# Performance work log

Hardware: AMD Instinct MI355X
Metric: run time of the kernel (lower is better)

Reference implementation:

```python
import jax, jax.numpy as jnp
import numpy as np

N_NODES = 100000
N_EDGES = 1600000
IN_CH = 64
HID = 64
OUT = 2


def sage_conv(x, src, dst, W_agg, W_root, b):
    # PyG SAGEConv (mean aggr): out = lin_l(mean_{j in N(i)} x_j) + lin_r(x_i)
    n = x.shape[0]
    msgs = x[src]                                        # [E, F] gather
    agg = jax.ops.segment_sum(msgs, dst, num_segments=n)  # [N, F] scatter-add
    cnt = jax.ops.segment_sum(jnp.ones((src.shape[0], 1), x.dtype), dst, num_segments=n)
    agg = agg / jnp.maximum(cnt, 1)                      # mean; isolated nodes -> 0
    return agg @ W_agg + x @ W_root + b


def setup_inputs() -> dict:
    key = jax.random.key(0)
    ks = jax.random.split(key, 8)
    s = lambda f: 1.0 / np.sqrt(f)
    x = jax.random.normal(ks[0], (N_NODES, IN_CH), dtype=jnp.float32)
    edge_index = jax.random.randint(ks[1], (2, N_EDGES), 0, N_NODES, dtype=jnp.int64)
    return {
        "x": x,
        "edge_index": edge_index,
        "W1_agg": jax.random.normal(ks[2], (IN_CH, HID), dtype=jnp.float32) * s(IN_CH),
        "W1_root": jax.random.normal(ks[3], (IN_CH, HID), dtype=jnp.float32) * s(IN_CH),
        "b1": jnp.zeros((HID,), jnp.float32),
        "W2_agg": jax.random.normal(ks[4], (HID, HID), dtype=jnp.float32) * s(HID),
        "W2_root": jax.random.normal(ks[5], (HID, HID), dtype=jnp.float32) * s(HID),
        "b2": jnp.zeros((HID,), jnp.float32),
        "W_lin": jax.random.normal(ks[6], (HID, OUT), dtype=jnp.float32) * s(HID),
        "b_lin": jnp.zeros((OUT,), jnp.float32),
    }


def reference(x, edge_index, W1_agg, W1_root, b1, W2_agg, W2_root, b2, W_lin, b_lin):
    src, dst = edge_index[0], edge_index[1]
    h = jax.nn.relu(sage_conv(x, src, dst, W1_agg, W1_root, b1))   # dropout = identity (eval)
    h = jax.nn.relu(sage_conv(h, src, dst, W2_agg, W2_root, b2))
    return h @ W_lin + b_lin
```

## Files before the change

kernel.cpp:

```cpp
#include <hip/hip_runtime.h>
#include <hip/hip_bf16.h>

#define FEAT 64
#define CHUNK 2048
#define MAX_NB 1024

typedef __attribute__((ext_vector_type(8))) short bf16x8;
typedef __attribute__((ext_vector_type(4))) float f32x4;
typedef __attribute__((ext_vector_type(2))) float f32x2;

__device__ __forceinline__ float bflo2f(unsigned int u) {
    union { unsigned int u; float f; } v; v.u = u << 16; return v.f;
}
__device__ __forceinline__ float bfhi2f(unsigned int u) {
    union { unsigned int u; float f; } v; v.u = u & 0xffff0000u; return v.f;
}
__device__ __forceinline__ unsigned short f2bf(float f) {
    union { float f; unsigned int u; } v; v.f = f;
    unsigned int u = v.u;
    u += 0x7fffu + ((u >> 16) & 1u);
    return (unsigned short)(u >> 16);
}
__device__ __forceinline__ f32x2 bfpair(unsigned int u) {
    f32x2 r; r.x = bflo2f(u & 0xffffu); r.y = bfhi2f(u); return r;
}

__global__ __launch_bounds__(256) void prep_p1_kernel(
    const unsigned short* __restrict__ xh, const int* __restrict__ ei32,
    const void* __restrict__ w1a, const void* __restrict__ w1r,
    const void* __restrict__ b1,  const void* __restrict__ w2a,
    const void* __restrict__ w2r, const void* __restrict__ b2,
    const void* __restrict__ wl,  const void* __restrict__ bl,
    float* __restrict__ wbuf, unsigned short* __restrict__ Wt,
    int* __restrict__ flags, const void* __restrict__ x_in,
    unsigned short* __restrict__ x16, int n8,
    int* __restrict__ hist, int E, int N, int NB, int EC, int pB) {
    __shared__ int lh[MAX_NB];
    __shared__ int cnt_bf, cnt_nz;
    int tid = threadIdx.x;

    if (blockIdx.x >= pB) {
        int c = blockIdx.x - pB;
        if (tid == 0) cnt_nz = 0;
        for (int i = tid; i < NB; i += 256) lh[i] = 0;
        __syncthreads();
        if (ei32[tid * 2 + 1] != 0) atomicAdd(&cnt_nz, 1);
        __syncthreads();
        int idx64 = (cnt_nz < 8) ? 1 : 0;
        long base = (long)c * CHUNK;
#pragma unroll 4
        for (int j = 0; j < CHUNK / 256; ++j) {
            long e = base + j * 256 + tid;
            if (e < E) {
                int d = idx64 ? ei32[2 * ((long)E + e)] : ei32[(long)E + e];
                if ((unsigned)d < (unsigned)N)
                    atomicAdd(&lh[d >> 8], 1);
            }
        }
        __syncthreads();
        for (int k = tid; k < NB; k += 256) hist[(long)k * EC + c] = lh[k];
        return;
    }

    if (tid == 0) { cnt_bf = 0; cnt_nz = 0; }
    __syncthreads();
    unsigned short h = xh[tid * 2];
    int e = (h >> 7) & 0xFF;
    if (e >= 110 && e <= 132) atomicAdd(&cnt_bf, 1);
    if (ei32[tid * 2 + 1] != 0) atomicAdd(&cnt_nz, 1);
    __syncthreads();
    int f0 = (cnt_bf >= 128) ? 1 : 0;
    if (blockIdx.x == 0 && tid == 0) {
        flags[0] = f0;
        flags[1] = (cnt_nz < 8) ? 1 : 0;
    }
    int i = blockIdx.x * 256 + tid;
    if (i < 16642) {
        const void* src; int off;
        if      (i < 4096)  { src = w1a; off = i; }
        else if (i < 8192)  { src = w1r; off = i - 4096; }
        else if (i < 8256)  { src = b1;  off = i - 8192; }
        else if (i < 12352) { src = w2a; off = i - 8256; }
        else if (i < 16448) { src = w2r; off = i - 12352; }
        else if (i < 16512) { src = b2;  off = i - 16448; }
        else if (i < 16640) { src = wl;  off = i - 16512; }
        else                { src = bl;  off = i - 16640; }
        float v = f0 ? bflo2f(((const unsigned short*)src)[off])
                     : ((const float*)src)[off];
        wbuf[i] = v;
        unsigned short hv = f2bf(v);
        if (i < 4096)                      Wt[(off & 63) * 128 + (off >> 6)] = hv;
        else if (i < 8192)                 Wt[(off & 63) * 128 + 64 + (off >> 6)] = hv;
        else if (i >= 8256 && i < 12352)   Wt[8192 + (off & 63) * 128 + (off >> 6)] = hv;
        else if (i >= 12352 && i < 16448)  Wt[8192 + (off & 63) * 128 + 64 + (off >> 6)] = hv;
    }
    if (!f0 && i < n8) {
        float4 a = ((const float4*)x_in)[2 * i];
        float4 b = ((const float4*)x_in)[2 * i + 1];
        uint4 o;
        o.x = (unsigned int)f2bf(a.x) | ((unsigned int)f2bf(a.y) << 16);
        o.y = (unsigned int)f2bf(a.z) | ((unsigned int)f2bf(a.w) << 16);
        o.z = (unsigned int)f2bf(b.x) | ((unsigned int)f2bf(b.y) << 16);
        o.w = (unsigned int)f2bf(b.z) | ((unsigned int)f2bf(b.w) << 16);
        ((uint4*)x16)[i] = o;
    }
}

__global__ __launch_bounds__(256) void scan1_kernel(const int* __restrict__ in,
                                                    int* __restrict__ out,
                                                    int* __restrict__ blocksum, int n) {
    int tid = threadIdx.x;
    int base = blockIdx.x * 2048 + tid * 8;
    int v[8];
    int tsum = 0;
#pragma unroll
    for (int i = 0; i < 8; ++i) {
        v[i] = (base + i < n) ? in[base + i] : 0;
        tsum += v[i];
    }
    int lane = tid & 63;
    int x = tsum;
#pragma unroll
    for (int off = 1; off < 64; off <<= 1) {
        int y = __shfl_up(x, off);
        if (lane >= off) x += y;
    }
    __shared__ int wsum[4];
    int wave = tid >> 6;
    if (lane == 63) wsum[wave] = x;
    __syncthreads();
    int woff = 0;
#pragma unroll
    for (int w = 0; w < 4; ++w) if (w < wave) woff += wsum[w];
    int run = woff + x - tsum;
#pragma unroll
    for (int i = 0; i < 8; ++i) {
        if (base + i < n) out[base + i] = run;
        run += v[i];
    }
    if (tid == 255) blocksum[blockIdx.x] = woff + x;
}

__global__ __launch_bounds__(256) void scan3_kernel(int* __restrict__ out,
                                                    const int* __restrict__ blocksum, int n) {
    int bb = blockIdx.x, tid = threadIdx.x;
    __shared__ int wsum[4];
    __shared__ int spre;
    int s = 0;
    for (int b = tid; b < bb; b += 256) s += blocksum[b];
#pragma unroll
    for (int off = 32; off > 0; off >>= 1) s += __shfl_down(s, off);
    int lane = tid & 63, wave = tid >> 6;
    if (lane == 0) wsum[wave] = s;
    __syncthreads();
    if (tid == 0) spre = wsum[0] + wsum[1] + wsum[2] + wsum[3];
    __syncthreads();
    int pre = spre;
    int base = bb * 2048;
#pragma unroll
    for (int k = 0; k < 8; ++k) {
        int i = base + k * 256 + tid;
        if (i < n) out[i] += pre;
    }
}

__global__ __launch_bounds__(256) void p3_scatter_kernel(
    const int* __restrict__ ei32, const int* __restrict__ hscan,
    int* __restrict__ bkt, int E, int N, int NB, int EC,
    const int* __restrict__ flags) {
    __shared__ int lh[MAX_NB];
    int tid = threadIdx.x, c = blockIdx.x;
    for (int i = tid; i < NB; i += 256) lh[i] = 0;
    __syncthreads();
    int idx64 = flags[1];
    long base = (long)c * CHUNK;
#pragma unroll 4
    for (int j = 0; j < CHUNK / 256; ++j) {
        long e = base + j * 256 + tid;
        if (e < E) {
            int s = idx64 ? ei32[2 * e]             : ei32[e];
            int d = idx64 ? ei32[2 * ((long)E + e)] : ei32[(long)E + e];
            if ((unsigned)d < (unsigned)N) {
                if ((unsigned)s >= (unsigned)N) s = 0;
                int k = d >> 8;
                int r = atomicAdd(&lh[k], 1);
                bkt[hscan[(long)k * EC + c] + r] = s | ((d & 255) << 20);
            }
        }
    }
}

__global__ __launch_bounds__(256) void p4_build_kernel(
    const int* __restrict__ bkt, const int* __restrict__ hscan, const int* __restrict__ hist,
    int* __restrict__ offs, int* __restrict__ cnt, int* __restrict__ srcs,
    int E, int N, int NB, int EC) {
    int k = blockIdx.x, tid = threadIdx.x;
    int start = hscan[(long)k * EC];
    int end = (k + 1 < NB) ? hscan[(long)(k + 1) * EC]
                           : (hscan[(long)NB * EC - 1] + hist[(long)NB * EC - 1]);
    __shared__ int lc[256], lheads[256], wsum[4];
    lc[tid] = 0;
    __syncthreads();
    for (int e = start + tid; e < end; e += 256)
        atomicAdd(&lc[(bkt[e] >> 20) & 255], 1);
    __syncthreads();
    int cv = lc[tid];
    int lane = tid & 63, wave = tid >> 6;
    int x = cv;
#pragma unroll
    for (int off = 1; off < 64; off <<= 1) {
        int y = __shfl_up(x, off);
        if (lane >= off) x += y;
    }
    if (lane == 63) wsum[wave] = x;
    __syncthreads();
    int woff = 0;
#pragma unroll
    for (int w = 0; w < 4; ++w) if (w < wave) woff += wsum[w];
    int excl = woff + x - cv;
    int gnode = k * 256 + tid;
    if (gnode < N) { offs[gnode] = start + excl; cnt[gnode] = cv; }
    lheads[tid] = excl;
    __syncthreads();
    for (int e = start + tid; e < end; e += 256) {
        int p = bkt[e];
        int d8 = (p >> 20) & 255;
        int pos = start + atomicAdd(&lheads[d8], 1);
        srcs[pos] = p & 0xFFFFF;
    }
}

__global__ __launch_bounds__(256) void sage_fused_kernel(
    const void* __restrict__ feat_raw, const unsigned short* __restrict__ feat_ws,
    const int* __restrict__ srcs, const int* __restrict__ offs,
    const int* __restrict__ cnt,
    const unsigned short* __restrict__ Wt, const float* __restrict__ bias,
    unsigned short* __restrict__ out16, int N,
    const float* __restrict__ wl, const float* __restrict__ bl,
    void* __restrict__ out_final, const int* __restrict__ flags, int sel) {

    const unsigned short* feat16 =
        (sel && !flags[0]) ? feat_ws : (const unsigned short*)feat_raw;

    __shared__ unsigned short A_l[64][72];
    __shared__ unsigned short B_l[64][136];

    int tid = threadIdx.x;
    int blk = blockIdx.x;

#pragma unroll
    for (int i = 0; i < 4; ++i) {
        int ch = tid + i * 256;
        int n = ch >> 4, kc = ch & 15;
        *(uint4*)&B_l[n][kc * 8] = *(const uint4*)(Wt + n * 128 + kc * 8);
    }

    int lane = tid & 63;
    int wave = tid >> 6;
    int g = lane >> 3;
    int li = lane & 7;

    for (int pass = 0; pass < 2; ++pass) {
        int r = pass * 32 + wave * 8 + g;
        int node = blk * 64 + r;
        f32x2 a0 = {0.f, 0.f}, a1 = a0, a2 = a0, a3 = a0;
        int deg = 0;
        if (node < N) {
            int start = offs[node];
            deg = cnt[node];
            int j = 0;
            for (; j + 4 <= deg; j += 4) {
                int s0 = srcs[start + j];
                int s1 = srcs[start + j + 1];
                int s2 = srcs[start + j + 2];
                int s3 = srcs[start + j + 3];
                uint4 u0 = *(const uint4*)(feat16 + (size_t)s0 * FEAT + 8 * li);
                uint4 u1 = *(const uint4*)(feat16 + (size_t)s1 * FEAT + 8 * li);
                uint4 u2 = *(const uint4*)(feat16 + (size_t)s2 * FEAT + 8 * li);
                uint4 u3 = *(const uint4*)(feat16 + (size_t)s3 * FEAT + 8 * li);
                a0 += bfpair(u0.x); a1 += bfpair(u0.y); a2 += bfpair(u0.z); a3 += bfpair(u0.w);
                a0 += bfpair(u1.x); a1 += bfpair(u1.y); a2 += bfpair(u1.z); a3 += bfpair(u1.w);
                a0 += bfpair(u2.x); a1 += bfpair(u2.y); a2 += bfpair(u2.z); a3 += bfpair(u2.w);
                a0 += bfpair(u3.x); a1 += bfpair(u3.y); a2 += bfpair(u3.z); a3 += bfpair(u3.w);
            }
            for (; j < deg; ++j) {
                int s = srcs[start + j];
                uint4 u = *(const uint4*)(feat16 + (size_t)s * FEAT + 8 * li);
                a0 += bfpair(u.x); a1 += bfpair(u.y); a2 += bfpair(u.z); a3 += bfpair(u.w);
            }
        }
        float inv = 1.0f / (float)(deg > 0 ? deg : 1);
        uint4 o;
        o.x = (unsigned)f2bf(a0.x * inv) | ((unsigned)f2bf(a0.y * inv) << 16);
        o.y = (unsigned)f2bf(a1.x * inv) | ((unsigned)f2bf(a1.y * inv) << 16);
        o.z = (unsigned)f2bf(a2.x * inv) | ((unsigned)f2bf(a2.y * inv) << 16);
        o.w = (unsigned)f2bf(a3.x * inv) | ((unsigned)f2bf(a3.y * inv) << 16);
        *(uint4*)&A_l[r][8 * li] = o;
    }
    __syncthreads();

    int r0 = wave * 16;
    int m = lane & 15, quad = lane >> 4;

    int arow = blk * 64 + r0 + m;
    if (arow >= N) arow = 0;
    const unsigned short* rootp = feat16 + (size_t)arow * FEAT + quad * 8;

    f32x4 acc0 = {0.f, 0.f, 0.f, 0.f};
    f32x4 acc1 = acc0, acc2 = acc0, acc3 = acc0;

#pragma unroll
    for (int k0 = 0; k0 < 128; k0 += 32) {
        bf16x8 a;
        if (k0 < 64) a = *(const bf16x8*)&A_l[r0 + m][k0 + quad * 8];
        else         a = *(const bf16x8*)(rootp + (k0 - 64));
        bf16x8 b0 = *(const bf16x8*)&B_l[ 0 + m][k0 + quad * 8];
        bf16x8 b1 = *(const bf16x8*)&B_l[16 + m][k0 + quad * 8];
        bf16x8 b2 = *(const bf16x8*)&B_l[32 + m][k0 + quad * 8];
        bf16x8 b3 = *(const bf16x8*)&B_l[48 + m][k0 + quad * 8];
        acc0 = __builtin_amdgcn_mfma_f32_16x16x32_bf16(a, b0, acc0, 0, 0, 0);
        acc1 = __builtin_amdgcn_mfma_f32_16x16x32_bf16(a, b1, acc1, 0, 0, 0);
        acc2 = __builtin_amdgcn_mfma_f32_16x16x32_bf16(a, b2, acc2, 0, 0, 0);
        acc3 = __builtin_amdgcn_mfma_f32_16x16x32_bf16(a, b3, acc3, 0, 0, 0);
    }
    __syncthreads();

#pragma unroll
    for (int c = 0; c < 4; ++c) {
        f32x4 av = (c == 0) ? acc0 : (c == 1) ? acc1 : (c == 2) ? acc2 : acc3;
        float bv = bias[c * 16 + m];
#pragma unroll
        for (int reg = 0; reg < 4; ++reg) {
            float v = fmaxf(av[reg] + bv, 0.f);
            A_l[r0 + quad * 4 + reg][c * 16 + m] = f2bf(v);
        }
    }
    __syncthreads();

    if (out16) {
#pragma unroll
        for (int i = 0; i < 2; ++i) {
            int ch = tid + i * 256;
            int r = ch >> 3, c = ch & 7;
            int row = blk * 64 + r;
            if (row < N)
                ((uint4*)(out16 + (size_t)row * FEAT))[c] = *(const uint4*)&A_l[r][c * 8];
        }
    }

    if (wl) {
        int r = tid >> 2, part = tid & 3;
        int row = blk * 64 + r;
        if (row < N) {
            float p0 = 0.f, p1 = 0.f;
#pragma unroll
            for (int j = 0; j < 16; ++j) {
                int f = part * 16 + j;
                float v = bflo2f(A_l[r][f]);
                p0 += v * wl[f * 2 + 0];
                p1 += v * wl[f * 2 + 1];
            }
            p0 += __shfl_down(p0, 2, 4); p0 += __shfl_down(p0, 1, 4);
            p1 += __shfl_down(p1, 2, 4); p1 += __shfl_down(p1, 1, 4);
            if (part == 0) {
                p0 += bl[0];
                p1 += bl[1];
                if (flags[0]) {
                    unsigned int o = ((unsigned int)f2bf(p1) << 16) | (unsigned int)f2bf(p0);
                    ((unsigned int*)out_final)[row] = o;
                } else {
                    ((float2*)out_final)[row] = make_float2(p0, p1);
                }
            }
        }
    }
}

extern "C" void kernel_launch(void* const* d_in, const int* in_sizes, int n_in,
                              void* d_out, int out_size, void* d_ws, size_t ws_size,
                              hipStream_t stream) {
    const void* x_in = d_in[0];
    const int*  ei32 = (const int*)d_in[1];

    int N = in_sizes[0] / FEAT;
    int E = in_sizes[1] / 2;
    int NB = (N + 255) >> 8;
    int EC = (E + CHUNK - 1) / CHUNK;
    int HN = NB * EC;

    unsigned short* x16   = (unsigned short*)d_ws;
    unsigned short* h16   = x16 + (size_t)N * FEAT;
    unsigned short* Wt    = h16 + (size_t)N * FEAT;
    float*          wbuf  = (float*)(Wt + 16384);
    int*            hist  = (int*)(wbuf + 16704);
    int*            hscan = hist + HN;
    int*            bsum  = hscan + HN;
    int*            flags = bsum + 1024;
    int*            offs  = flags + 16;
    int*            cnt   = offs + N;
    int*            bkt   = cnt + N;
    int*            srcs  = bkt + E;

    float* b1_32 = wbuf + 8192;
    float* b2_32 = wbuf + 16448;
    float* wl32  = wbuf + 16512;
    float* bl32  = wbuf + 16640;

    int n8 = N * FEAT / 8;
    int pBlocks = (n8 + 255) / 256;
    if (pBlocks < 66) pBlocks = 66;
    prep_p1_kernel<<<pBlocks + EC, 256, 0, stream>>>(
        (const unsigned short*)x_in, ei32,
        d_in[2], d_in[3], d_in[4], d_in[5], d_in[6], d_in[7], d_in[8], d_in[9],
        wbuf, Wt, flags, x_in, x16, n8,
        hist, E, N, NB, EC, pBlocks);

    int sB = (HN + 2047) / 2048;
    scan1_kernel<<<sB, 256, 0, stream>>>(hist, hscan, bsum, HN);
    scan3_kernel<<<sB, 256, 0, stream>>>(hscan, bsum, HN);
    p3_scatter_kernel<<<EC, 256, 0, stream>>>(ei32, hscan, bkt, E, N, NB, EC, flags);
    p4_build_kernel<<<NB, 256, 0, stream>>>(bkt, hscan, hist, offs, cnt, srcs, E, N, NB, EC);

    int gBlocks = (N + 63) / 64;

    sage_fused_kernel<<<gBlocks, 256, 0, stream>>>(
        x_in, x16, srcs, offs, cnt, Wt, b1_32, h16, N,
        nullptr, nullptr, nullptr, flags, 1);

    sage_fused_kernel<<<gBlocks, 256, 0, stream>>>(
        h16, h16, srcs, offs, cnt, Wt + 8192, b2_32, nullptr, N,
        wl32, bl32, d_out, flags, 0);
}
```

Before: 231.4 us.

## Replace two-level bucket CSR build with global atomic count and scatter

Replaces the bucketed histogram, scatter and per-bucket build passes with a direct per-node degree count using global atomics, a scan over node counts, and a single atomic-cursor scatter of source indices. This removes one kernel launch and the intermediate bucket array. In exchange it issues global atomics per edge twice onto random addresses, and the neighbour order within each node becomes nondeterministic, which can change floating-point summation order.

Measured after the change: 400.8 us. 1.73x slower.

```diff
diff --git a/kernel.cpp b/kernel.cpp
--- a/kernel.cpp
+++ b/kernel.cpp
@@ -2,8 +2,7 @@
 #include <hip/hip_bf16.h>
 
 #define FEAT 64
-#define CHUNK 2048
-#define MAX_NB 1024
+#define CHUNK 8192
 
 typedef __attribute__((ext_vector_type(8))) short bf16x8;
 typedef __attribute__((ext_vector_type(4))) float f32x4;
@@ -25,7 +24,7 @@
     f32x2 r; r.x = bflo2f(u & 0xffffu); r.y = bfhi2f(u); return r;
 }
 
-__global__ __launch_bounds__(256) void prep_p1_kernel(
+__global__ __launch_bounds__(256) void prep_count_kernel(
     const unsigned short* __restrict__ xh, const int* __restrict__ ei32,
     const void* __restrict__ w1a, const void* __restrict__ w1r,
     const void* __restrict__ b1,  const void* __restrict__ w2a,
@@ -34,15 +33,13 @@
     float* __restrict__ wbuf, unsigned short* __restrict__ Wt,
     int* __restrict__ flags, const void* __restrict__ x_in,
     unsigned short* __restrict__ x16, int n8,
-    int* __restrict__ hist, int E, int N, int NB, int EC, int pB) {
-    __shared__ int lh[MAX_NB];
+    int* __restrict__ cnt_g, int E, int N, int pB) {
     __shared__ int cnt_bf, cnt_nz;
     int tid = threadIdx.x;
 
     if (blockIdx.x >= pB) {
         int c = blockIdx.x - pB;
         if (tid == 0) cnt_nz = 0;
-        for (int i = tid; i < NB; i += 256) lh[i] = 0;
         __syncthreads();
         if (ei32[tid * 2 + 1] != 0) atomicAdd(&cnt_nz, 1);
         __syncthreads();
@@ -54,11 +51,9 @@
             if (e < E) {
                 int d = idx64 ? ei32[2 * ((long)E + e)] : ei32[(long)E + e];
                 if ((unsigned)d < (unsigned)N)
-                    atomicAdd(&lh[d >> 8], 1);
-            }
-        }
-        __syncthreads();
-        for (int k = tid; k < NB; k += 256) hist[(long)k * EC + c] = lh[k];
+                    atomicAdd(&cnt_g[d], 1);
+            }
+        }
         return;
     }
 
@@ -142,6 +137,7 @@
 }
 
 __global__ __launch_bounds__(256) void scan3_kernel(int* __restrict__ out,
+                                                    int* __restrict__ head,
                                                     const int* __restrict__ blocksum, int n) {
     int bb = blockIdx.x, tid = threadIdx.x;
     __shared__ int wsum[4];
@@ -160,73 +156,27 @@
 #pragma unroll
     for (int k = 0; k < 8; ++k) {
         int i = base + k * 256 + tid;
-        if (i < n) out[i] += pre;
-    }
-}
-
-__global__ __launch_bounds__(256) void p3_scatter_kernel(
-    const int* __restrict__ ei32, const int* __restrict__ hscan,
-    int* __restrict__ bkt, int E, int N, int NB, int EC,
-    const int* __restrict__ flags) {
-    __shared__ int lh[MAX_NB];
-    int tid = threadIdx.x, c = blockIdx.x;
-    for (int i = tid; i < NB; i += 256) lh[i] = 0;
-    __syncthreads();
+        if (i < n) {
+            int v = out[i] + pre;
+            out[i] = v;
+            head[i] = v;
+        }
+    }
+}
+
+__global__ __launch_bounds__(256) void scatter_kernel(
+    const int* __restrict__ ei32, int* __restrict__ head,
+    int* __restrict__ srcs, int E, int N, const int* __restrict__ flags) {
     int idx64 = flags[1];
-    long base = (long)c * CHUNK;
-#pragma unroll 4
-    for (int j = 0; j < CHUNK / 256; ++j) {
-        long e = base + j * 256 + tid;
-        if (e < E) {
-            int s = idx64 ? ei32[2 * e]             : ei32[e];
-            int d = idx64 ? ei32[2 * ((long)E + e)] : ei32[(long)E + e];
-            if ((unsigned)d < (unsigned)N) {
-                if ((unsigned)s >= (unsigned)N) s = 0;
-                int k = d >> 8;
-                int r = atomicAdd(&lh[k], 1);
-                bkt[hscan[(long)k * EC + c] + r] = s | ((d & 255) << 20);
-            }
-        }
-    }
-}
-
-__global__ __launch_bounds__(256) void p4_build_kernel(
-    const int* __restrict__ bkt, const int* __restrict__ hscan, const int* __restrict__ hist,
-    int* __restrict__ offs, int* __restrict__ cnt, int* __restrict__ srcs,
-    int E, int N, int NB, int EC) {
-    int k = blockIdx.x, tid = threadIdx.x;
-    int start = hscan[(long)k * EC];
-    int end = (k + 1 < NB) ? hscan[(long)(k + 1) * EC]
-                           : (hscan[(long)NB * EC - 1] + hist[(long)NB * EC - 1]);
-    __shared__ int lc[256], lheads[256], wsum[4];
-    lc[tid] = 0;
-    __syncthreads();
-    for (int e = start + tid; e < end; e += 256)
-        atomicAdd(&lc[(bkt[e] >> 20) & 255], 1);
-    __syncthreads();
-    int cv = lc[tid];
-    int lane = tid & 63, wave = tid >> 6;
-    int x = cv;
-#pragma unroll
-    for (int off = 1; off < 64; off <<= 1) {
-        int y = __shfl_up(x, off);
-        if (lane >= off) x += y;
-    }
-    if (lane == 63) wsum[wave] = x;
-    __syncthreads();
-    int woff = 0;
-#pragma unroll
-    for (int w = 0; w < 4; ++w) if (w < wave) woff += wsum[w];
-    int excl = woff + x - cv;
-    int gnode = k * 256 + tid;
-    if (gnode < N) { offs[gnode] = start + excl; cnt[gnode] = cv; }
-    lheads[tid] = excl;
-    __syncthreads();
-    for (int e = start + tid; e < end; e += 256) {
-        int p = bkt[e];
-        int d8 = (p >> 20) & 255;
-        int pos = start + atomicAdd(&lheads[d8], 1);
-        srcs[pos] = p & 0xFFFFF;
+    long stride = (long)gridDim.x * 256;
+    for (long e = (long)blockIdx.x * 256 + threadIdx.x; e < E; e += stride) {
+        int s = idx64 ? ei32[2 * e]             : ei32[e];
+        int d = idx64 ? ei32[2 * ((long)E + e)] : ei32[(long)E + e];
+        if ((unsigned)d < (unsigned)N) {
+            if ((unsigned)s >= (unsigned)N) s = 0;
+            int pos = atomicAdd(&head[d], 1);
+            srcs[pos] = s;
+        }
     }
 }
 
@@ -384,42 +334,42 @@
 
     int N = in_sizes[0] / FEAT;
     int E = in_sizes[1] / 2;
-    int NB = (N + 255) >> 8;
-    int EC = (E + CHUNK - 1) / CHUNK;
-    int HN = NB * EC;
 
     unsigned short* x16   = (unsigned short*)d_ws;
     unsigned short* h16   = x16 + (size_t)N * FEAT;
     unsigned short* Wt    = h16 + (size_t)N * FEAT;
     float*          wbuf  = (float*)(Wt + 16384);
-    int*            hist  = (int*)(wbuf + 16704);
-    int*            hscan = hist + HN;
-    int*            bsum  = hscan + HN;
-    int*            flags = bsum + 1024;
-    int*            offs  = flags + 16;
-    int*            cnt   = offs + N;
-    int*            bkt   = cnt + N;
-    int*            srcs  = bkt + E;
+    int*            flags = (int*)(wbuf + 16704);
+    int*            bsum  = flags + 16;
+    int*            cnt   = bsum + 1024;
+    int*            offs  = cnt + N;
+    int*            head  = offs + N;
+    int*            srcs  = head + N;
 
     float* b1_32 = wbuf + 8192;
     float* b2_32 = wbuf + 16448;
     float* wl32  = wbuf + 16512;
     float* bl32  = wbuf + 16640;
 
+    hipMemsetAsync(cnt, 0, (size_t)N * sizeof(int), stream);
+
     int n8 = N * FEAT / 8;
     int pBlocks = (n8 + 255) / 256;
     if (pBlocks < 66) pBlocks = 66;
-    prep_p1_kernel<<<pBlocks + EC, 256, 0, stream>>>(
+    int cB = (E + CHUNK - 1) / CHUNK;
+    prep_count_kernel<<<pBlocks + cB, 256, 0, stream>>>(
         (const unsigned short*)x_in, ei32,
         d_in[2], d_in[3], d_in[4], d_in[5], d_in[6], d_in[7], d_in[8], d_in[9],
         wbuf, Wt, flags, x_in, x16, n8,
-        hist, E, N, NB, EC, pBlocks);
-
-    int sB = (HN + 2047) / 2048;
-    scan1_kernel<<<sB, 256, 0, stream>>>(hist, hscan, bsum, HN);
-    scan3_kernel<<<sB, 256, 0, stream>>>(hscan, bsum, HN);
-    p3_scatter_kernel<<<EC, 256, 0, stream>>>(ei32, hscan, bkt, E, N, NB, EC, flags);
-    p4_build_kernel<<<NB, 256, 0, stream>>>(bkt, hscan, hist, offs, cnt, srcs, E, N, NB, EC);
+        cnt, E, N, pBlocks);
+
+    int sB = (N + 2047) / 2048;
+    scan1_kernel<<<sB, 256, 0, stream>>>(cnt, offs, bsum, N);
+    scan3_kernel<<<sB, 256, 0, stream>>>(offs, head, bsum, N);
+
+    int scB = (E + 255) / 256;
+    if (scB > 2048) scB = 2048;
+    scatter_kernel<<<scB, 256, 0, stream>>>(ei32, head, srcs, E, N, flags);
 
     int gBlocks = (N + 63) / 64;
 
```

## Merge CSR-building kernels into one cooperative kernel with grid syncs

Applied to the files above, without the earlier changes.

The five CSR-construction launches (prep/histogram, two scan passes, bucket scatter, per-bucket build) are replaced by a single cooperative kernel on a fixed 512-block grid, with grid-wide syncs between phases. The aim is to remove launch gaps and tail effects between the small dependent kernels. A fallback path of separate kernels runs if the cooperative launch is unavailable. In exchange, the persistent grid loops over chunks with fewer blocks than before (EC is about 782 chunks), grid.sync has its own cost, and the unroll pragmas were dropped.

Result: slower. 511.9 us (+121.2%).

```diff
diff --git a/kernel.cpp b/kernel.cpp
--- a/kernel.cpp
+++ b/kernel.cpp
@@ -1,9 +1,13 @@
 #include <hip/hip_runtime.h>
 #include <hip/hip_bf16.h>
+#include <hip/hip_cooperative_groups.h>
 
 #define FEAT 64
 #define CHUNK 2048
 #define MAX_NB 1024
+#define MEGA_GRID 512
+
+namespace cg = cooperative_groups;
 
 typedef __attribute__((ext_vector_type(8))) short bf16x8;
 typedef __attribute__((ext_vector_type(4))) float f32x4;
@@ -25,56 +29,13 @@
     f32x2 r; r.x = bflo2f(u & 0xffffu); r.y = bfhi2f(u); return r;
 }
 
-__global__ __launch_bounds__(256) void prep_p1_kernel(
-    const unsigned short* __restrict__ xh, const int* __restrict__ ei32,
-    const void* __restrict__ w1a, const void* __restrict__ w1r,
-    const void* __restrict__ b1,  const void* __restrict__ w2a,
-    const void* __restrict__ w2r, const void* __restrict__ b2,
-    const void* __restrict__ wl,  const void* __restrict__ bl,
-    float* __restrict__ wbuf, unsigned short* __restrict__ Wt,
-    int* __restrict__ flags, const void* __restrict__ x_in,
-    unsigned short* __restrict__ x16, int n8,
-    int* __restrict__ hist, int E, int N, int NB, int EC, int pB) {
-    __shared__ int lh[MAX_NB];
-    __shared__ int cnt_bf, cnt_nz;
-    int tid = threadIdx.x;
-
-    if (blockIdx.x >= pB) {
-        int c = blockIdx.x - pB;
-        if (tid == 0) cnt_nz = 0;
-        for (int i = tid; i < NB; i += 256) lh[i] = 0;
-        __syncthreads();
-        if (ei32[tid * 2 + 1] != 0) atomicAdd(&cnt_nz, 1);
-        __syncthreads();
-        int idx64 = (cnt_nz < 8) ? 1 : 0;
-        long base = (long)c * CHUNK;
-#pragma unroll 4
-        for (int j = 0; j < CHUNK / 256; ++j) {
-            long e = base + j * 256 + tid;
-            if (e < E) {
-                int d = idx64 ? ei32[2 * ((long)E + e)] : ei32[(long)E + e];
-                if ((unsigned)d < (unsigned)N)
-                    atomicAdd(&lh[d >> 8], 1);
-            }
-        }
-        __syncthreads();
-        for (int k = tid; k < NB; k += 256) hist[(long)k * EC + c] = lh[k];
-        return;
-    }
-
-    if (tid == 0) { cnt_bf = 0; cnt_nz = 0; }
-    __syncthreads();
-    unsigned short h = xh[tid * 2];
-    int e = (h >> 7) & 0xFF;
-    if (e >= 110 && e <= 132) atomicAdd(&cnt_bf, 1);
-    if (ei32[tid * 2 + 1] != 0) atomicAdd(&cnt_nz, 1);
-    __syncthreads();
-    int f0 = (cnt_bf >= 128) ? 1 : 0;
-    if (blockIdx.x == 0 && tid == 0) {
-        flags[0] = f0;
-        flags[1] = (cnt_nz < 8) ? 1 : 0;
-    }
-    int i = blockIdx.x * 256 + tid;
+
+__device__ __forceinline__ void phase_prep_elem(
+    int i, int f0,
+    const void* w1a, const void* w1r, const void* b1, const void* w2a,
+    const void* w2r, const void* b2, const void* wl, const void* bl,
+    float* wbuf, unsigned short* Wt,
+    const void* x_in, unsigned short* x16, int n8) {
     if (i < 16642) {
         const void* src; int off;
         if      (i < 4096)  { src = w1a; off = i; }
@@ -106,18 +67,32 @@
     }
 }
 
-__global__ __launch_bounds__(256) void scan1_kernel(const int* __restrict__ in,
-                                                    int* __restrict__ out,
-                                                    int* __restrict__ blocksum, int n) {
-    int tid = threadIdx.x;
-    int base = blockIdx.x * 2048 + tid * 8;
+__device__ __forceinline__ void phase_hist_chunk(
+    int c, int idx64, const int* __restrict__ ei32, int* __restrict__ hist,
+    int E, int N, int NB, int EC, int* lh, int tid) {
+    for (int i = tid; i < NB; i += 256) lh[i] = 0;
+    __syncthreads();
+    long base = (long)c * CHUNK;
+    for (int j = 0; j < CHUNK / 256; ++j) {
+        long e = base + j * 256 + tid;
+        if (e < E) {
+            int d = idx64 ? ei32[2 * ((long)E + e)] : ei32[(long)E + e];
+            if ((unsigned)d < (unsigned)N) atomicAdd(&lh[d >> 8], 1);
+        }
+    }
+    __syncthreads();
+    for (int k = tid; k < NB; k += 256) hist[(long)k * EC + c] = lh[k];
+    __syncthreads();
+}
+
+__device__ __forceinline__ void phase_scan1_block(
+    int b, const int* __restrict__ in, int* __restrict__ out,
+    int* __restrict__ bsum, int n, int tid, int* sh) {
+    int base = b * 2048 + tid * 8;
     int v[8];
     int tsum = 0;
 #pragma unroll
-    for (int i = 0; i < 8; ++i) {
-        v[i] = (base + i < n) ? in[base + i] : 0;
-        tsum += v[i];
-    }
+    for (int i = 0; i < 8; ++i) { v[i] = (base + i < n) ? in[base + i] : 0; tsum += v[i]; }
     int lane = tid & 63;
     int x = tsum;
 #pragma unroll
@@ -125,56 +100,47 @@
         int y = __shfl_up(x, off);
         if (lane >= off) x += y;
     }
-    __shared__ int wsum[4];
     int wave = tid >> 6;
-    if (lane == 63) wsum[wave] = x;
+    if (lane == 63) sh[wave] = x;
     __syncthreads();
     int woff = 0;
 #pragma unroll
-    for (int w = 0; w < 4; ++w) if (w < wave) woff += wsum[w];
+    for (int w = 0; w < 4; ++w) if (w < wave) woff += sh[w];
     int run = woff + x - tsum;
 #pragma unroll
-    for (int i = 0; i < 8; ++i) {
-        if (base + i < n) out[base + i] = run;
-        run += v[i];
-    }
-    if (tid == 255) blocksum[blockIdx.x] = woff + x;
-}
-
-__global__ __launch_bounds__(256) void scan3_kernel(int* __restrict__ out,
-                                                    const int* __restrict__ blocksum, int n) {
-    int bb = blockIdx.x, tid = threadIdx.x;
-    __shared__ int wsum[4];
-    __shared__ int spre;
+    for (int i = 0; i < 8; ++i) { if (base + i < n) out[base + i] = run; run += v[i]; }
+    if (tid == 255) bsum[b] = woff + x;
+    __syncthreads();
+}
+
+__device__ __forceinline__ void phase_scan3_block(
+    int b, int* __restrict__ out, const int* __restrict__ bsum,
+    int n, int tid, int* sh) {
     int s = 0;
-    for (int b = tid; b < bb; b += 256) s += blocksum[b];
+    for (int q = tid; q < b; q += 256) s += bsum[q];
 #pragma unroll
     for (int off = 32; off > 0; off >>= 1) s += __shfl_down(s, off);
     int lane = tid & 63, wave = tid >> 6;
-    if (lane == 0) wsum[wave] = s;
-    __syncthreads();
-    if (tid == 0) spre = wsum[0] + wsum[1] + wsum[2] + wsum[3];
-    __syncthreads();
-    int pre = spre;
-    int base = bb * 2048;
+    if (lane == 0) sh[wave] = s;
+    __syncthreads();
+    if (tid == 0) sh[4] = sh[0] + sh[1] + sh[2] + sh[3];
+    __syncthreads();
+    int pre = sh[4];
+    int base = b * 2048;
 #pragma unroll
     for (int k = 0; k < 8; ++k) {
         int i = base + k * 256 + tid;
         if (i < n) out[i] += pre;
     }
-}
-
-__global__ __launch_bounds__(256) void p3_scatter_kernel(
-    const int* __restrict__ ei32, const int* __restrict__ hscan,
-    int* __restrict__ bkt, int E, int N, int NB, int EC,
-    const int* __restrict__ flags) {
-    __shared__ int lh[MAX_NB];
-    int tid = threadIdx.x, c = blockIdx.x;
+    __syncthreads();
+}
+
+__device__ __forceinline__ void phase_p3_chunk(
+    int c, int idx64, const int* __restrict__ ei32, const int* __restrict__ hscan,
+    int* __restrict__ bkt, int E, int N, int NB, int EC, int* lh, int tid) {
     for (int i = tid; i < NB; i += 256) lh[i] = 0;
     __syncthreads();
-    int idx64 = flags[1];
     long base = (long)c * CHUNK;
-#pragma unroll 4
     for (int j = 0; j < CHUNK / 256; ++j) {
         long e = base + j * 256 + tid;
         if (e < E) {
@@ -188,17 +154,17 @@
             }
         }
     }
-}
-
-__global__ __launch_bounds__(256) void p4_build_kernel(
-    const int* __restrict__ bkt, const int* __restrict__ hscan, const int* __restrict__ hist,
-    int* __restrict__ offs, int* __restrict__ cnt, int* __restrict__ srcs,
-    int E, int N, int NB, int EC) {
-    int k = blockIdx.x, tid = threadIdx.x;
+    __syncthreads();
+}
+
+__device__ __forceinline__ void phase_p4_bucket(
+    int k, const int* __restrict__ bkt, const int* __restrict__ hscan,
+    const int* __restrict__ hist, int* __restrict__ offs, int* __restrict__ cnt,
+    int* __restrict__ srcs, int N, int NB, int EC, int* sh, int tid) {
+    int* lc = sh; int* lheads = sh + 256; int* wsum = sh + 512;
     int start = hscan[(long)k * EC];
     int end = (k + 1 < NB) ? hscan[(long)(k + 1) * EC]
                            : (hscan[(long)NB * EC - 1] + hist[(long)NB * EC - 1]);
-    __shared__ int lc[256], lheads[256], wsum[4];
     lc[tid] = 0;
     __syncthreads();
     for (int e = start + tid; e < end; e += 256)
@@ -228,6 +194,105 @@
         int pos = start + atomicAdd(&lheads[d8], 1);
         srcs[pos] = p & 0xFFFFF;
     }
+    __syncthreads();
+}
+
+__global__ __launch_bounds__(256) void csr_mega_kernel(
+    const unsigned short* __restrict__ xh, const int* __restrict__ ei32,
+    const void* w1a, const void* w1r, const void* b1, const void* w2a,
+    const void* w2r, const void* b2, const void* wl, const void* bl,
+    float* __restrict__ wbuf, unsigned short* __restrict__ Wt, int* __restrict__ flags,
+    const void* __restrict__ x_in, unsigned short* __restrict__ x16, int n8, int pMax,
+    int* __restrict__ hist, int* __restrict__ hscan, int* __restrict__ bsum,
+    int* __restrict__ offs, int* __restrict__ cnt, int* __restrict__ bkt,
+    int* __restrict__ srcs,
+    int E, int N, int NB, int EC, int HN, int sB) {
+    cg::grid_group grid = cg::this_grid();
+    __shared__ int sh[MAX_NB];
+    int tid = threadIdx.x;
+
+    if (tid == 0) { sh[0] = 0; sh[1] = 0; }
+    __syncthreads();
+    if (ei32[tid * 2 + 1] != 0) atomicAdd(&sh[0], 1);
+    { unsigned short h = xh[tid * 2]; int e = (h >> 7) & 0xFF;
+      if (e >= 110 && e <= 132) atomicAdd(&sh[1], 1); }
+    __syncthreads();
+    int idx64 = (sh[0] < 8) ? 1 : 0;
+    int f0 = (sh[1] >= 128) ? 1 : 0;
+    if (blockIdx.x == 0 && tid == 0) { flags[0] = f0; flags[1] = idx64; }
+    __syncthreads();
+
+    for (int i = blockIdx.x * 256 + tid; i < pMax; i += gridDim.x * 256)
+        phase_prep_elem(i, f0, w1a, w1r, b1, w2a, w2r, b2, wl, bl,
+                        wbuf, Wt, x_in, x16, n8);
+
+    for (int c = blockIdx.x; c < EC; c += gridDim.x)
+        phase_hist_chunk(c, idx64, ei32, hist, E, N, NB, EC, sh, tid);
+    grid.sync();
+
+    if (blockIdx.x < sB) phase_scan1_block(blockIdx.x, hist, hscan, bsum, HN, tid, sh);
+    grid.sync();
+
+    if (blockIdx.x < sB) phase_scan3_block(blockIdx.x, hscan, bsum, HN, tid, sh);
+    grid.sync();
+
+    for (int c = blockIdx.x; c < EC; c += gridDim.x)
+        phase_p3_chunk(c, idx64, ei32, hscan, bkt, E, N, NB, EC, sh, tid);
+    grid.sync();
+
+    for (int k = blockIdx.x; k < NB; k += gridDim.x)
+        phase_p4_bucket(k, bkt, hscan, hist, offs, cnt, srcs, N, NB, EC, sh, tid);
+}
+
+__global__ __launch_bounds__(256) void fb_prep_kernel(
+    const unsigned short* __restrict__ xh, const int* __restrict__ ei32,
+    const void* w1a, const void* w1r, const void* b1, const void* w2a,
+    const void* w2r, const void* b2, const void* wl, const void* bl,
+    float* __restrict__ wbuf, unsigned short* __restrict__ Wt, int* __restrict__ flags,
+    const void* __restrict__ x_in, unsigned short* __restrict__ x16, int n8, int pMax) {
+    __shared__ int c0, c1;
+    int tid = threadIdx.x;
+    if (tid == 0) { c0 = 0; c1 = 0; }
+    __syncthreads();
+    if (ei32[tid * 2 + 1] != 0) atomicAdd(&c0, 1);
+    { unsigned short h = xh[tid * 2]; int e = (h >> 7) & 0xFF;
+      if (e >= 110 && e <= 132) atomicAdd(&c1, 1); }
+    __syncthreads();
+    int f0 = (c1 >= 128) ? 1 : 0;
+    if (blockIdx.x == 0 && tid == 0) { flags[0] = f0; flags[1] = (c0 < 8) ? 1 : 0; }
+    int i = blockIdx.x * 256 + tid;
+    if (i < pMax)
+        phase_prep_elem(i, f0, w1a, w1r, b1, w2a, w2r, b2, wl, bl,
+                        wbuf, Wt, x_in, x16, n8);
+}
+__global__ __launch_bounds__(256) void fb_hist_kernel(
+    const int* __restrict__ ei32, int* __restrict__ hist,
+    int E, int N, int NB, int EC, const int* __restrict__ flags) {
+    __shared__ int sh[MAX_NB];
+    phase_hist_chunk(blockIdx.x, flags[1], ei32, hist, E, N, NB, EC, sh, threadIdx.x);
+}
+__global__ __launch_bounds__(256) void fb_scan1_kernel(
+    const int* __restrict__ in, int* __restrict__ out, int* __restrict__ bsum, int n) {
+    __shared__ int sh[8];
+    phase_scan1_block(blockIdx.x, in, out, bsum, n, threadIdx.x, sh);
+}
+__global__ __launch_bounds__(256) void fb_scan3_kernel(
+    int* __restrict__ out, const int* __restrict__ bsum, int n) {
+    __shared__ int sh[8];
+    phase_scan3_block(blockIdx.x, out, bsum, n, threadIdx.x, sh);
+}
+__global__ __launch_bounds__(256) void fb_p3_kernel(
+    const int* __restrict__ ei32, const int* __restrict__ hscan, int* __restrict__ bkt,
+    int E, int N, int NB, int EC, const int* __restrict__ flags) {
+    __shared__ int sh[MAX_NB];
+    phase_p3_chunk(blockIdx.x, flags[1], ei32, hscan, bkt, E, N, NB, EC, sh, threadIdx.x);
+}
+__global__ __launch_bounds__(256) void fb_p4_kernel(
+    const int* __restrict__ bkt, const int* __restrict__ hscan,
+    const int* __restrict__ hist, int* __restrict__ offs, int* __restrict__ cnt,
+    int* __restrict__ srcs, int N, int NB, int EC) {
+    __shared__ int sh[520];
+    phase_p4_bucket(blockIdx.x, bkt, hscan, hist, offs, cnt, srcs, N, NB, EC, sh, threadIdx.x);
 }
 
 __global__ __launch_bounds__(256) void sage_fused_kernel(
@@ -381,12 +446,18 @@
                               hipStream_t stream) {
     const void* x_in = d_in[0];
     const int*  ei32 = (const int*)d_in[1];
+    const unsigned short* xh = (const unsigned short*)x_in;
+    const void* w1a = d_in[2]; const void* w1r = d_in[3];
+    const void* b1p = d_in[4]; const void* w2a = d_in[5];
+    const void* w2r = d_in[6]; const void* b2p = d_in[7];
+    const void* wlp = d_in[8]; const void* blp = d_in[9];
 
     int N = in_sizes[0] / FEAT;
     int E = in_sizes[1] / 2;
     int NB = (N + 255) >> 8;
     int EC = (E + CHUNK - 1) / CHUNK;
     int HN = NB * EC;
+    int sB = (HN + 2047) / 2048;
 
     unsigned short* x16   = (unsigned short*)d_ws;
     unsigned short* h16   = x16 + (size_t)N * FEAT;
@@ -407,19 +478,36 @@
     float* bl32  = wbuf + 16640;
 
     int n8 = N * FEAT / 8;
-    int pBlocks = (n8 + 255) / 256;
-    if (pBlocks < 66) pBlocks = 66;
-    prep_p1_kernel<<<pBlocks + EC, 256, 0, stream>>>(
-        (const unsigned short*)x_in, ei32,
-        d_in[2], d_in[3], d_in[4], d_in[5], d_in[6], d_in[7], d_in[8], d_in[9],
-        wbuf, Wt, flags, x_in, x16, n8,
-        hist, E, N, NB, EC, pBlocks);
-
-    int sB = (HN + 2047) / 2048;
-    scan1_kernel<<<sB, 256, 0, stream>>>(hist, hscan, bsum, HN);
-    scan3_kernel<<<sB, 256, 0, stream>>>(hscan, bsum, HN);
-    p3_scatter_kernel<<<EC, 256, 0, stream>>>(ei32, hscan, bkt, E, N, NB, EC, flags);
-    p4_build_kernel<<<NB, 256, 0, stream>>>(bkt, hscan, hist, offs, cnt, srcs, E, N, NB, EC);
+    int pMax = (n8 > 16642) ? n8 : 16642;
+
+    bool coop = false;
+    int occ = 0;
+    if (hipOccupancyMaxActiveBlocksPerMultiprocessor(&occ, csr_mega_kernel, 256, 0)
+            == hipSuccess && occ >= 2) {
+        void* args[] = {
+            (void*)&xh, (void*)&ei32,
+            (void*)&w1a, (void*)&w1r, (void*)&b1p, (void*)&w2a,
+            (void*)&w2r, (void*)&b2p, (void*)&wlp, (void*)&blp,
+            (void*)&wbuf, (void*)&Wt, (void*)&flags,
+            (void*)&x_in, (void*)&x16, (void*)&n8, (void*)&pMax,
+            (void*)&hist, (void*)&hscan, (void*)&bsum,
+            (void*)&offs, (void*)&cnt, (void*)&bkt, (void*)&srcs,
+            (void*)&E, (void*)&N, (void*)&NB, (void*)&EC, (void*)&HN, (void*)&sB };
+        if (hipLaunchCooperativeKernel(csr_mega_kernel, dim3(MEGA_GRID), dim3(256),
+                                       args, 0, stream) == hipSuccess)
+            coop = true;
+    }
+    if (!coop) {
+        int pBlocks = (pMax + 255) / 256;
+        fb_prep_kernel<<<pBlocks, 256, 0, stream>>>(
+            xh, ei32, w1a, w1r, b1p, w2a, w2r, b2p, wlp, blp,
+            wbuf, Wt, flags, x_in, x16, n8, pMax);
+        fb_hist_kernel<<<EC, 256, 0, stream>>>(ei32, hist, E, N, NB, EC, flags);
+        fb_scan1_kernel<<<sB, 256, 0, stream>>>(hist, hscan, bsum, HN);
+        fb_scan3_kernel<<<sB, 256, 0, stream>>>(hscan, bsum, HN);
+        fb_p3_kernel<<<EC, 256, 0, stream>>>(ei32, hscan, bkt, E, N, NB, EC, flags);
+        fb_p4_kernel<<<NB, 256, 0, stream>>>(bkt, hscan, hist, offs, cnt, srcs, N, NB, EC);
+    }
 
     int gBlocks = (N + 63) / 64;
 
```

## Merge two-pass histogram scan into single-pass chained scan, enlarge edge chunks

Applied to the files above, without the earlier changes.

Replaces the two scan kernels with one kernel in which each block publishes its block total through a flag and spins on all earlier blocks' flags to build its prefix. This removes one kernel launch and a second pass over the histogram. The edge chunk size grows from 2048 to 8192, so there are four times fewer histogram columns and scatter blocks, but each block does more serial work and has less parallelism. The chained scan assumes earlier blocks get scheduled first; with the small grid this is likely safe, but it is a forward-progress risk.

Result: slower. 243.7 us (+5.3%).

```diff
diff --git a/kernel.cpp b/kernel.cpp
--- a/kernel.cpp
+++ b/kernel.cpp
@@ -2,7 +2,7 @@
 #include <hip/hip_bf16.h>
 
 #define FEAT 64
-#define CHUNK 2048
+#define CHUNK 8192
 #define MAX_NB 1024
 
 typedef __attribute__((ext_vector_type(8))) short bf16x8;
@@ -34,7 +34,8 @@
     float* __restrict__ wbuf, unsigned short* __restrict__ Wt,
     int* __restrict__ flags, const void* __restrict__ x_in,
     unsigned short* __restrict__ x16, int n8,
-    int* __restrict__ hist, int E, int N, int NB, int EC, int pB) {
+    int* __restrict__ hist, int* __restrict__ bflag, int sB,
+    int E, int N, int NB, int EC, int pB) {
     __shared__ int lh[MAX_NB];
     __shared__ int cnt_bf, cnt_nz;
     int tid = threadIdx.x;
@@ -70,9 +71,12 @@
     if (ei32[tid * 2 + 1] != 0) atomicAdd(&cnt_nz, 1);
     __syncthreads();
     int f0 = (cnt_bf >= 128) ? 1 : 0;
-    if (blockIdx.x == 0 && tid == 0) {
-        flags[0] = f0;
-        flags[1] = (cnt_nz < 8) ? 1 : 0;
+    if (blockIdx.x == 0) {
+        if (tid == 0) {
+            flags[0] = f0;
+            flags[1] = (cnt_nz < 8) ? 1 : 0;
+        }
+        if (tid < sB) bflag[tid] = 0;
     }
     int i = blockIdx.x * 256 + tid;
     if (i < 16642) {
@@ -106,11 +110,11 @@
     }
 }
 
-__global__ __launch_bounds__(256) void scan1_kernel(const int* __restrict__ in,
-                                                    int* __restrict__ out,
-                                                    int* __restrict__ blocksum, int n) {
-    int tid = threadIdx.x;
-    int base = blockIdx.x * 2048 + tid * 8;
+__global__ __launch_bounds__(256) void scan_kernel(
+    const int* __restrict__ in, int* __restrict__ out,
+    int* __restrict__ bsum, int* __restrict__ bflag, int n) {
+    int b = blockIdx.x, tid = threadIdx.x;
+    int base = b * 2048 + tid * 8;
     int v[8];
     int tsum = 0;
 #pragma unroll
@@ -126,10 +130,28 @@
         if (lane >= off) x += y;
     }
     __shared__ int wsum[4];
+    __shared__ int spre;
     int wave = tid >> 6;
     if (lane == 63) wsum[wave] = x;
     __syncthreads();
-    int woff = 0;
+    if (tid == 255) {
+        int total = 0;
+#pragma unroll
+        for (int w = 0; w < 4; ++w) total += wsum[w];
+        atomicExch(&bsum[b], total);
+        __threadfence();
+        atomicExch(&bflag[b], 1);
+    }
+    if (tid == 0) {
+        int pre = 0;
+        for (int q = 0; q < b; ++q) {
+            while (atomicAdd(&bflag[q], 0) == 0) { }
+            pre += atomicAdd(&bsum[q], 0);
+        }
+        spre = pre;
+    }
+    __syncthreads();
+    int woff = spre;
 #pragma unroll
     for (int w = 0; w < 4; ++w) if (w < wave) woff += wsum[w];
     int run = woff + x - tsum;
@@ -137,30 +159,6 @@
     for (int i = 0; i < 8; ++i) {
         if (base + i < n) out[base + i] = run;
         run += v[i];
-    }
-    if (tid == 255) blocksum[blockIdx.x] = woff + x;
-}
-
-__global__ __launch_bounds__(256) void scan3_kernel(int* __restrict__ out,
-                                                    const int* __restrict__ blocksum, int n) {
-    int bb = blockIdx.x, tid = threadIdx.x;
-    __shared__ int wsum[4];
-    __shared__ int spre;
-    int s = 0;
-    for (int b = tid; b < bb; b += 256) s += blocksum[b];
-#pragma unroll
-    for (int off = 32; off > 0; off >>= 1) s += __shfl_down(s, off);
-    int lane = tid & 63, wave = tid >> 6;
-    if (lane == 0) wsum[wave] = s;
-    __syncthreads();
-    if (tid == 0) spre = wsum[0] + wsum[1] + wsum[2] + wsum[3];
-    __syncthreads();
-    int pre = spre;
-    int base = bb * 2048;
-#pragma unroll
-    for (int k = 0; k < 8; ++k) {
-        int i = base + k * 256 + tid;
-        if (i < n) out[i] += pre;
     }
 }
 
@@ -387,6 +385,7 @@
     int NB = (N + 255) >> 8;
     int EC = (E + CHUNK - 1) / CHUNK;
     int HN = NB * EC;
+    int sB = (HN + 2047) / 2048;
 
     unsigned short* x16   = (unsigned short*)d_ws;
     unsigned short* h16   = x16 + (size_t)N * FEAT;
@@ -395,7 +394,8 @@
     int*            hist  = (int*)(wbuf + 16704);
     int*            hscan = hist + HN;
     int*            bsum  = hscan + HN;
-    int*            flags = bsum + 1024;
+    int*            bflag = bsum + 512;
+    int*            flags = bflag + 512;
     int*            offs  = flags + 16;
     int*            cnt   = offs + N;
     int*            bkt   = cnt + N;
@@ -413,11 +413,9 @@
         (const unsigned short*)x_in, ei32,
         d_in[2], d_in[3], d_in[4], d_in[5], d_in[6], d_in[7], d_in[8], d_in[9],
         wbuf, Wt, flags, x_in, x16, n8,
-        hist, E, N, NB, EC, pBlocks);
-
-    int sB = (HN + 2047) / 2048;
-    scan1_kernel<<<sB, 256, 0, stream>>>(hist, hscan, bsum, HN);
-    scan3_kernel<<<sB, 256, 0, stream>>>(hscan, bsum, HN);
+        hist, bflag, sB, E, N, NB, EC, pBlocks);
+
+    scan_kernel<<<sB, 256, 0, stream>>>(hist, hscan, bsum, bflag, HN);
     p3_scatter_kernel<<<EC, 256, 0, stream>>>(ei32, hscan, bkt, E, N, NB, EC, flags);
     p4_build_kernel<<<NB, 256, 0, stream>>>(bkt, hscan, hist, offs, cnt, srcs, E, N, NB, EC);
 
```
